# Kernel tuning notes

Measured on AMD Instinct MI355X. Metric: run time of the kernel, lower is better.

The kernel has to match this reference:

```python
import jax, jax.numpy as jnp
import numpy as np

N = 200_000          # active voxels
CIN, COUT = 64, 128  # in_filters, out_filters
GRID = (32, 480, 480)  # sparse spatial shape (D, H, W)
NEG_SLOPE = 0.01     # nn.LeakyReLU default
EPS = 1e-5           # BatchNorm1d default


def _build_nbrs():
    """Build rulebook-style neighbor tables for the two submanifold kernels.

    Returns nbr31 [9, N] for kernel (3,1,3) and nbr13 [9, N] for kernel (1,3,3).
    Entry == N means 'no active neighbor' (maps to a zero pad row).
    """
    rng = np.random.default_rng(0)
    prod = GRID[0] * GRID[1] * GRID[2]
    lin = rng.choice(prod, size=N, replace=False)
    z, y, x = np.unravel_index(lin, GRID)
    lut = np.full(prod, N, dtype=np.int64)
    lut[lin] = np.arange(N)

    def nbrs(offsets):
        out = np.full((len(offsets), N), N, dtype=np.int32)
        for k, (dz, dy, dx) in enumerate(offsets):
            zz, yy, xx = z + dz, y + dy, x + dx
            valid = ((zz >= 0) & (zz < GRID[0]) & (yy >= 0) & (yy < GRID[1])
                     & (xx >= 0) & (xx < GRID[2]))
            l2 = (zz * GRID[1] + yy) * GRID[2] + xx
            out[k, valid] = lut[l2[valid]].astype(np.int32)
        return out

    off31 = [(dz, 0, dx) for dz in (-1, 0, 1) for dx in (-1, 0, 1)]  # (3,1,3)
    off13 = [(0, dy, dx) for dy in (-1, 0, 1) for dx in (-1, 0, 1)]  # (1,3,3)
    return nbrs(off31), nbrs(off13)


def setup_inputs() -> dict:
    key = jax.random.key(0)
    ks = jax.random.split(key, 5)
    nbr31, nbr13 = _build_nbrs()
    s_in = (2.0 / (9 * CIN)) ** 0.5
    s_out = (2.0 / (9 * COUT)) ** 0.5
    ones = jnp.ones((COUT,), jnp.float32)
    zeros = jnp.zeros((COUT,), jnp.float32)
    return {
        "feats": jax.random.normal(ks[0], (N, CIN), jnp.float32),
        "W1": jax.random.normal(ks[1], (9, CIN, COUT), jnp.float32) * s_in,
        "W1_2": jax.random.normal(ks[2], (9, COUT, COUT), jnp.float32) * s_out,
        "W2": jax.random.normal(ks[3], (9, CIN, COUT), jnp.float32) * s_in,
        "W3": jax.random.normal(ks[4], (9, COUT, COUT), jnp.float32) * s_out,
        "g0": ones, "b0": zeros,      # bn0  (init: weight=1, bias=0)
        "g0_2": ones, "b0_2": zeros,  # bn0_2
        "g1": ones, "b1": zeros,      # bn1
        "g2": ones, "b2": zeros,      # bn2
        "nbr31": jnp.asarray(nbr31),
        "nbr13": jnp.asarray(nbr13),
    }


def _subm_conv(f, W, nbr):
    # f [N, Cin], W [9, Cin, Cout], nbr [9, N] -> [N, Cout]
    fp = jnp.concatenate([f, jnp.zeros((1, f.shape[1]), f.dtype)], axis=0)
    g = fp[nbr]  # gather: [9, N, Cin]
    return jnp.einsum("knc,kcd->nd", g, W)


def _lrelu(f):
    return jnp.where(f >= 0, f, NEG_SLOPE * f)


def _bn(f, gamma, beta):
    # BatchNorm1d training-mode batch stats (biased variance) over voxel dim
    m = jnp.mean(f, axis=0)
    v = jnp.mean(jnp.square(f), axis=0) - m * m
    return (f - m) * jax.lax.rsqrt(v + EPS) * gamma + beta


def reference(feats, W1, W1_2, W2, W3, g0, b0, g0_2, b0_2, g1, b1, g2, b2,
              nbr31, nbr13):
    shortcut = _bn(_lrelu(_subm_conv(feats, W1, nbr31)), g0, b0)
    shortcut = _bn(_lrelu(_subm_conv(shortcut, W1_2, nbr13)), g0_2, b0_2)
    resA = _bn(_lrelu(_subm_conv(feats, W2, nbr13)), g1, b1)
    resA = _bn(_lrelu(_subm_conv(resA, W3, nbr31)), g2, b2)
    return resA + shortcut
```

## Files before the change

kernel.cpp:

```cpp
#include <hip/hip_runtime.h>

#define NV 200000
#define NCH 391
#define PCAP 56
#define SNB 256

typedef __attribute__((ext_vector_type(8))) short sh8;
typedef __attribute__((ext_vector_type(4))) float f32x4;
typedef __attribute__((ext_vector_type(2))) unsigned int u32x2;

__device__ inline unsigned short f2bf(float f) {
  unsigned int u = __builtin_bit_cast(unsigned int, f);
  u += 0x7FFFu + ((u >> 16) & 1u);
  return (unsigned short)(u >> 16);
}
__device__ inline float bf2f(unsigned short h) {
  unsigned int u = ((unsigned int)h) << 16;
  return __builtin_bit_cast(float, u);
}
__device__ inline float lrelu(float v) { return v >= 0.f ? v : 0.01f * v; }

__global__ __launch_bounds__(256) void prep_k(
    const float* __restrict__ W1, const float* __restrict__ W12,
    const float* __restrict__ W2, const float* __restrict__ W3,
    unsigned short* __restrict__ T1, unsigned short* __restrict__ T12,
    unsigned short* __restrict__ T2, unsigned short* __restrict__ T3,
    const int* __restrict__ nbr31, const int* __restrict__ nbr13,
    int2* __restrict__ pairs, int* __restrict__ cc) {
  __shared__ int base_s[4];
  __shared__ int run;
  int bx = blockIdx.x;
  if (bx < 1728) {
    int i = bx * 256 + threadIdx.x;
    const float* src;
    unsigned short* dst;
    int cin;
    if (i < 73728) {
      src = W1; dst = T1; cin = 64;
    } else if (i < 147456) {
      src = W2; dst = T2; cin = 64; i -= 73728;
    } else if (i < 294912) {
      src = W12; dst = T12; cin = 128; i -= 147456;
    } else {
      src = W3; dst = T3; cin = 128; i -= 294912;
    }
    const int c = i % cin;
    const int rest = i / cin;
    const int d = rest % 128;
    const int k = rest / 128;
    dst[i] = f2bf(src[((size_t)(k * cin + c)) * 128 + d]);
    return;
  }
  bx -= 1728;
  const int slot = bx / NCH, chunk = bx % NCH;
  const int table = slot >> 3, kk = slot & 7;
  const int k = kk + (kk >= 4);
  const int* nb = (table ? nbr13 : nbr31) + (size_t)k * NV;
  const int tid = threadIdx.x, lane = tid & 63, wv = tid >> 6;
  if (tid == 0) run = 0;
  __syncthreads();
  int2* pw = pairs + (size_t)(slot * NCH + chunk) * PCAP;
#pragma unroll
  for (int i = 0; i < 2; ++i) {
    const int n = chunk * 512 + i * 256 + tid;
    const int val = (n < NV) ? nb[n] : NV;
    const bool valid = (val != NV);
    const unsigned long long m = __ballot(valid);
    const int loff = __popcll(m & ((1ull << lane) - 1ull));
    if (lane == 0) base_s[wv] = __popcll(m);
    __syncthreads();
    int wbase = run;
    for (int w = 0; w < wv; ++w) wbase += base_s[w];
    if (valid) {
      const int pos = wbase + loff;
      if (pos < PCAP) {
        int2 pr;
        pr.x = val;
        pr.y = n;
        pw[pos] = pr;
      }
    }
    __syncthreads();
    if (tid == 0) run += base_s[0] + base_s[1] + base_s[2] + base_s[3];
    __syncthreads();
  }
  if (tid == 0) cc[slot * NCH + chunk] = min(run, PCAP);
}

__global__ __launch_bounds__(256) void center2_k(
    const float* __restrict__ X, const unsigned short* __restrict__ W1t,
    const unsigned short* __restrict__ W2t, unsigned short* __restrict__ Y1,
    unsigned short* __restrict__ Y2) {
  constexpr int CIN = 64, CH = 8;
  __shared__ unsigned short tile[64 * CIN];
  const int tid = threadIdx.x, lane = tid & 63, wv = tid >> 6;
  const int l15 = lane & 15, l4 = lane >> 4;
  const int row0 = blockIdx.x * 64;
  const int js = tid & 7;
#pragma unroll
  for (int i = 0; i < 2; ++i) {
    const int u = i * 256 + tid;
    const int r = u >> 3;
    const f32x4 a = *(const f32x4*)(X + (size_t)(row0 + r) * CIN + js * 8);
    const f32x4 b = *(const f32x4*)(X + (size_t)(row0 + r) * CIN + js * 8 + 4);
    sh8 o;
#pragma unroll
    for (int j = 0; j < 4; ++j) {
      o[j] = (short)f2bf(a[j]);
      o[4 + j] = (short)f2bf(b[j]);
    }
    *(sh8*)(tile + ((size_t)r * CH + (js ^ (r & 7))) * 8) = o;
  }
  __syncthreads();

  f32x4 acc1[2][4], acc2[2][4];
#pragma unroll
  for (int mt = 0; mt < 2; ++mt)
#pragma unroll
    for (int nt = 0; nt < 4; ++nt) {
      acc1[mt][nt] = (f32x4){0.f, 0.f, 0.f, 0.f};
      acc2[mt][nt] = (f32x4){0.f, 0.f, 0.f, 0.f};
    }
  const unsigned short* W1K = W1t + (size_t)(4 * 128) * CIN;
  const unsigned short* W2K = W2t + (size_t)(4 * 128) * CIN;
#pragma unroll
  for (int s = 0; s < 2; ++s) {
    sh8 aw1[2], aw2[2];
#pragma unroll
    for (int mt = 0; mt < 2; ++mt) {
      const int d = (wv * 2 + mt) * 16 + l15;
      aw1[mt] = *(const sh8*)(W1K + (size_t)d * CIN + s * 32 + l4 * 8);
      aw2[mt] = *(const sh8*)(W2K + (size_t)d * CIN + s * 32 + l4 * 8);
    }
#pragma unroll
    for (int nt = 0; nt < 4; ++nt) {
      const int r = nt * 16 + l15;
      const int j = s * 4 + l4;
      const sh8 bx = *(const sh8*)(tile + ((size_t)r * CH + (j ^ (r & 7))) * 8);
#pragma unroll
      for (int mt = 0; mt < 2; ++mt) {
        acc1[mt][nt] =
            __builtin_amdgcn_mfma_f32_16x16x32_bf16(aw1[mt], bx, acc1[mt][nt], 0, 0, 0);
        acc2[mt][nt] =
            __builtin_amdgcn_mfma_f32_16x16x32_bf16(aw2[mt], bx, acc2[mt][nt], 0, 0, 0);
      }
    }
  }
#pragma unroll
  for (int mt = 0; mt < 2; ++mt)
#pragma unroll
    for (int nt = 0; nt < 4; ++nt) {
      const int n = row0 + nt * 16 + l15;
      const int d0 = (wv * 2 + mt) * 16 + l4 * 4;
      u32x2 p1, p2;
      p1[0] = (unsigned)f2bf(acc1[mt][nt][0]) | ((unsigned)f2bf(acc1[mt][nt][1]) << 16);
      p1[1] = (unsigned)f2bf(acc1[mt][nt][2]) | ((unsigned)f2bf(acc1[mt][nt][3]) << 16);
      p2[0] = (unsigned)f2bf(acc2[mt][nt][0]) | ((unsigned)f2bf(acc2[mt][nt][1]) << 16);
      p2[1] = (unsigned)f2bf(acc2[mt][nt][2]) | ((unsigned)f2bf(acc2[mt][nt][3]) << 16);
      *(u32x2*)(Y1 + (size_t)n * 128 + d0) = p1;
      *(u32x2*)(Y2 + (size_t)n * 128 + d0) = p2;
    }
}

__global__ __launch_bounds__(256) void c128_k(
    const unsigned short* __restrict__ X, const unsigned short* __restrict__ Wt,
    const float* __restrict__ abp, unsigned short* __restrict__ Y) {
  constexpr int CIN = 128, CH = 16;
  __shared__ unsigned short tile[64 * CIN];
  const int row0 = blockIdx.x * 64;
  const int tid = threadIdx.x, lane = tid & 63, wv = tid >> 6;
  const int l15 = lane & 15, l4 = lane >> 4;
  const int js = tid & 15;
  const f32x4 aL = *(const f32x4*)(abp + js * 8);
  const f32x4 aH = *(const f32x4*)(abp + js * 8 + 4);
  const f32x4 bL = *(const f32x4*)(abp + 128 + js * 8);
  const f32x4 bH = *(const f32x4*)(abp + 128 + js * 8 + 4);
#pragma unroll
  for (int i = 0; i < 4; ++i) {
    const int u = i * 256 + tid;
    const int r = u >> 4;
    const sh8 v = *(const sh8*)(X + (size_t)(row0 + r) * CIN + js * 8);
    sh8 o;
#pragma unroll
    for (int j = 0; j < 4; ++j) {
      o[j] = (short)f2bf(lrelu(bf2f((unsigned short)v[j])) * aL[j] + bL[j]);
      o[4 + j] = (short)f2bf(lrelu(bf2f((unsigned short)v[4 + j])) * aH[j] + bH[j]);
    }
    *(sh8*)(tile + ((size_t)r * CH + (js ^ (r & 7))) * 8) = o;
  }
  __syncthreads();

  f32x4 acc[2][4];
#pragma unroll
  for (int mt = 0; mt < 2; ++mt)
#pragma unroll
    for (int nt = 0; nt < 4; ++nt) acc[mt][nt] = (f32x4){0.f, 0.f, 0.f, 0.f};

  const unsigned short* WtK = Wt + (size_t)(4 * 128) * CIN;
#pragma unroll
  for (int s = 0; s < 4; ++s) {
    sh8 aw[2];
#pragma unroll
    for (int mt = 0; mt < 2; ++mt) {
      const int d = (wv * 2 + mt) * 16 + l15;
      aw[mt] = *(const sh8*)(WtK + (size_t)d * CIN + s * 32 + l4 * 8);
    }
#pragma unroll
    for (int nt = 0; nt < 4; ++nt) {
      const int r = nt * 16 + l15;
      const int j = s * 4 + l4;
      const sh8 bxv = *(const sh8*)(tile + ((size_t)r * CH + (j ^ (r & 7))) * 8);
#pragma unroll
      for (int mt = 0; mt < 2; ++mt)
        acc[mt][nt] =
            __builtin_amdgcn_mfma_f32_16x16x32_bf16(aw[mt], bxv, acc[mt][nt], 0, 0, 0);
    }
  }
#pragma unroll
  for (int mt = 0; mt < 2; ++mt)
#pragma unroll
    for (int nt = 0; nt < 4; ++nt) {
      const int n = row0 + nt * 16 + l15;
      const int d0 = (wv * 2 + mt) * 16 + l4 * 4;
      u32x2 pk;
      pk[0] = (unsigned)f2bf(acc[mt][nt][0]) | ((unsigned)f2bf(acc[mt][nt][1]) << 16);
      pk[1] = (unsigned)f2bf(acc[mt][nt][2]) | ((unsigned)f2bf(acc[mt][nt][3]) << 16);
      *(u32x2*)(Y + (size_t)n * 128 + d0) = pk;
    }
}

__global__ __launch_bounds__(256) void off64_k(
    const float* __restrict__ X, const unsigned short* __restrict__ T1,
    const unsigned short* __restrict__ T2, const int2* __restrict__ pairs,
    const int* __restrict__ cc, unsigned short* __restrict__ y1,
    unsigned short* __restrict__ y2) {
  constexpr int CIN = 64, CH = 8;
  const int layer = blockIdx.x / NCH, chunk = blockIdx.x % NCH;
  const unsigned short* Wt = layer ? T2 : T1;
  unsigned short* Y = layer ? y2 : y1;
  const int* ccl = cc + layer * 8 * NCH;
  const int2* pl = pairs + (size_t)layer * 8 * NCH * PCAP;
  __shared__ unsigned short tile[64 * CIN];
  __shared__ int sin[64], sout[64];
  const int tid = threadIdx.x, lane = tid & 63, wv = tid >> 6;
  const int l15 = lane & 15, l4 = lane >> 4;
  const int js = tid & 7;

  for (int kk = 0; kk < 8; ++kk) {
    const int n0 = ccl[kk * NCH + chunk];
    if (n0 == 0) continue;
    const int k = kk + (kk >= 4);
    const unsigned short* WtK = Wt + (size_t)k * 128 * CIN;
    __syncthreads();
    if (tid < 64) {
      int2 pr;
      if (tid < n0) pr = pl[(size_t)(kk * NCH + chunk) * PCAP + tid];
      else { pr.x = NV; pr.y = NV; }
      sin[tid] = pr.x;
      sout[tid] = pr.y;
    }
    __syncthreads();
#pragma unroll
    for (int i = 0; i < 2; ++i) {
      const int r = (i * 256 + tid) >> 3;
      const int in = sin[r];
      sh8 o = (sh8){0, 0, 0, 0, 0, 0, 0, 0};
      if (in != NV) {
        const f32x4 a = *(const f32x4*)(X + (size_t)in * CIN + js * 8);
        const f32x4 b = *(const f32x4*)(X + (size_t)in * CIN + js * 8 + 4);
#pragma unroll
        for (int j = 0; j < 4; ++j) {
          o[j] = (short)f2bf(a[j]);
          o[4 + j] = (short)f2bf(b[j]);
        }
      }
      *(sh8*)(tile + ((size_t)r * CH + (js ^ (r & 7))) * 8) = o;
    }
    __syncthreads();

    f32x4 acc[2][4];
#pragma unroll
    for (int mt = 0; mt < 2; ++mt)
#pragma unroll
      for (int nt = 0; nt < 4; ++nt) acc[mt][nt] = (f32x4){0.f, 0.f, 0.f, 0.f};
#pragma unroll
    for (int s = 0; s < 2; ++s) {
      sh8 aw[2];
#pragma unroll
      for (int mt = 0; mt < 2; ++mt) {
        const int d = (wv * 2 + mt) * 16 + l15;
        aw[mt] = *(const sh8*)(WtK + (size_t)d * CIN + s * 32 + l4 * 8);
      }
#pragma unroll
      for (int nt = 0; nt < 4; ++nt) {
        const int r = nt * 16 + l15;
        const int j = s * 4 + l4;
        const sh8 bxv = *(const sh8*)(tile + ((size_t)r * CH + (j ^ (r & 7))) * 8);
#pragma unroll
        for (int mt = 0; mt < 2; ++mt)
          acc[mt][nt] =
              __builtin_amdgcn_mfma_f32_16x16x32_bf16(aw[mt], bxv, acc[mt][nt], 0, 0, 0);
      }
    }
#pragma unroll
    for (int mt = 0; mt < 2; ++mt)
#pragma unroll
      for (int nt = 0; nt < 4; ++nt) {
        const int out = sout[nt * 16 + l15];
        if (out == NV) continue;
        const int d0 = (wv * 2 + mt) * 16 + l4 * 4;
        unsigned short* p = Y + (size_t)out * 128 + d0;
        const u32x2 old = *(const u32x2*)p;
        u32x2 nw;
        nw[0] = (unsigned)f2bf(bf2f((unsigned short)(old[0] & 0xffff)) + acc[mt][nt][0]) |
                ((unsigned)f2bf(bf2f((unsigned short)(old[0] >> 16)) + acc[mt][nt][1]) << 16);
        nw[1] = (unsigned)f2bf(bf2f((unsigned short)(old[1] & 0xffff)) + acc[mt][nt][2]) |
                ((unsigned)f2bf(bf2f((unsigned short)(old[1] >> 16)) + acc[mt][nt][3]) << 16);
        *(u32x2*)p = nw;
      }
  }
}

__global__ __launch_bounds__(256) void off128_k(
    const unsigned short* __restrict__ X, const unsigned short* __restrict__ Wt,
    const int2* __restrict__ pairs_t, const int* __restrict__ cc_t,
    const float* __restrict__ abp, unsigned short* __restrict__ Y) {
  constexpr int CIN = 128, CH = 16;
  const int chunk = blockIdx.x;
  __shared__ unsigned short tile[64 * CIN];
  __shared__ int sin[64], sout[64];
  const int tid = threadIdx.x, lane = tid & 63, wv = tid >> 6;
  const int l15 = lane & 15, l4 = lane >> 4;
  const int js = tid & 15;
  const f32x4 aL = *(const f32x4*)(abp + js * 8);
  const f32x4 aH = *(const f32x4*)(abp + js * 8 + 4);
  const f32x4 bL = *(const f32x4*)(abp + 128 + js * 8);
  const f32x4 bH = *(const f32x4*)(abp + 128 + js * 8 + 4);

  for (int kk = 0; kk < 8; ++kk) {
    const int n0 = cc_t[kk * NCH + chunk];
    if (n0 == 0) continue;
    const int k = kk + (kk >= 4);
    const unsigned short* WtK = Wt + (size_t)k * 128 * CIN;
    __syncthreads();
    if (tid < 64) {
      int2 pr;
      if (tid < n0) pr = pairs_t[(size_t)(kk * NCH + chunk) * PCAP + tid];
      else { pr.x = NV; pr.y = NV; }
      sin[tid] = pr.x;
      sout[tid] = pr.y;
    }
    __syncthreads();
#pragma unroll
    for (int i = 0; i < 4; ++i) {
      const int r = (i * 256 + tid) >> 4;
      const int in = sin[r];
      sh8 o = (sh8){0, 0, 0, 0, 0, 0, 0, 0};
      if (in != NV) {
        const sh8 v = *(const sh8*)(X + (size_t)in * CIN + js * 8);
#pragma unroll
        for (int j = 0; j < 4; ++j) {
          o[j] = (short)f2bf(lrelu(bf2f((unsigned short)v[j])) * aL[j] + bL[j]);
          o[4 + j] = (short)f2bf(lrelu(bf2f((unsigned short)v[4 + j])) * aH[j] + bH[j]);
        }
      }
      *(sh8*)(tile + ((size_t)r * CH + (js ^ (r & 7))) * 8) = o;
    }
    __syncthreads();

    f32x4 acc[2][4];
#pragma unroll
    for (int mt = 0; mt < 2; ++mt)
#pragma unroll
      for (int nt = 0; nt < 4; ++nt) acc[mt][nt] = (f32x4){0.f, 0.f, 0.f, 0.f};
#pragma unroll
    for (int s = 0; s < 4; ++s) {
      sh8 aw[2];
#pragma unroll
      for (int mt = 0; mt < 2; ++mt) {
        const int d = (wv * 2 + mt) * 16 + l15;
        aw[mt] = *(const sh8*)(WtK + (size_t)d * CIN + s * 32 + l4 * 8);
      }
#pragma unroll
      for (int nt = 0; nt < 4; ++nt) {
        const int r = nt * 16 + l15;
        const int j = s * 4 + l4;
        const sh8 bxv = *(const sh8*)(tile + ((size_t)r * CH + (j ^ (r & 7))) * 8);
#pragma unroll
        for (int mt = 0; mt < 2; ++mt)
          acc[mt][nt] =
              __builtin_amdgcn_mfma_f32_16x16x32_bf16(aw[mt], bxv, acc[mt][nt], 0, 0, 0);
      }
    }
#pragma unroll
    for (int mt = 0; mt < 2; ++mt)
#pragma unroll
      for (int nt = 0; nt < 4; ++nt) {
        const int out = sout[nt * 16 + l15];
        if (out == NV) continue;
        const int d0 = (wv * 2 + mt) * 16 + l4 * 4;
        unsigned short* p = Y + (size_t)out * 128 + d0;
        const u32x2 old = *(const u32x2*)p;
        u32x2 nw;
        nw[0] = (unsigned)f2bf(bf2f((unsigned short)(old[0] & 0xffff)) + acc[mt][nt][0]) |
                ((unsigned)f2bf(bf2f((unsigned short)(old[0] >> 16)) + acc[mt][nt][1]) << 16);
        nw[1] = (unsigned)f2bf(bf2f((unsigned short)(old[1] & 0xffff)) + acc[mt][nt][2]) |
                ((unsigned)f2bf(bf2f((unsigned short)(old[1] >> 16)) + acc[mt][nt][3]) << 16);
        *(u32x2*)p = nw;
      }
  }
}

__device__ inline void stats_body(const unsigned short* __restrict__ Y,
                                  float* __restrict__ partial, int b) {
  const int tid = threadIdx.x;
  float s[8], q[8];
#pragma unroll
  for (int j = 0; j < 8; ++j) { s[j] = 0.f; q[j] = 0.f; }
  for (long c = (long)b * 256 + tid; c < (long)NV * 16; c += (long)SNB * 256) {
    const sh8 v = *(const sh8*)(Y + c * 8);
#pragma unroll
    for (int j = 0; j < 8; ++j) {
      const float f = lrelu(bf2f((unsigned short)v[j]));
      s[j] += f;
      q[j] += f * f;
    }
  }
  __shared__ float red[256 * 16];
#pragma unroll
  for (int j = 0; j < 8; ++j) {
    red[tid * 16 + j] = s[j];
    red[tid * 16 + 8 + j] = q[j];
  }
  __syncthreads();
  if (tid < 128) {
    const int g = tid >> 3, j = tid & 7;
    float vs = 0.f, vq = 0.f;
#pragma unroll
    for (int i = 0; i < 16; ++i) {
      vs += red[(g + 16 * i) * 16 + j];
      vq += red[(g + 16 * i) * 16 + 8 + j];
    }
    partial[(size_t)b * 256 + tid] = vs;
    partial[(size_t)b * 256 + 128 + tid] = vq;
  }
}

__global__ __launch_bounds__(256) void stats2_k(const unsigned short* __restrict__ Y1,
                                                const unsigned short* __restrict__ Y2,
                                                float* __restrict__ P1,
                                                float* __restrict__ P2) {
  if (blockIdx.x < SNB) stats_body(Y1, P1, blockIdx.x);
  else stats_body(Y2, P2, blockIdx.x - SNB);
}

__global__ __launch_bounds__(1024) void fin2_k(
    const float* __restrict__ PA, const float* __restrict__ gA,
    const float* __restrict__ btA, float* __restrict__ abA,
    const float* __restrict__ PB, const float* __restrict__ gB,
    const float* __restrict__ btB, float* __restrict__ abB) {
  const float* P = blockIdx.x ? PB : PA;
  const float* g = blockIdx.x ? gB : gA;
  const float* bt = blockIdx.x ? btB : btA;
  float* abo = blockIdx.x ? abB : abA;
  __shared__ float S[1024];
  const int t = threadIdx.x;
  const int c = t & 255, grp = t >> 8;
  float s = 0.f;
#pragma unroll 8
  for (int b = grp * 64; b < grp * 64 + 64; ++b) s += P[(size_t)b * 256 + c];
  S[t] = s;
  __syncthreads();
  if (t < 256) S[t] = S[t] + S[256 + t] + S[512 + t] + S[768 + t];
  __syncthreads();
  if (t < 128) {
    const float m = S[t] * (1.0f / (float)NV);
    const float v = S[128 + t] * (1.0f / (float)NV) - m * m;
    const float a = g[t] * rsqrtf(v + 1e-5f);
    abo[t] = a;
    abo[128 + t] = bt[t] - m * a;
  }
}

__global__ __launch_bounds__(256) void final_k(const unsigned short* __restrict__ y3,
                                               const unsigned short* __restrict__ ysc,
                                               const float* __restrict__ ab3,
                                               const float* __restrict__ ab1,
                                               float* __restrict__ out) {
  const long i = (long)blockIdx.x * 256 + threadIdx.x;
  if (i >= (long)NV * 16) return;
  const long base = i * 8;
  const int c0 = (int)(base & 127);
  const sh8 v3 = *(const sh8*)(y3 + base);
  const sh8 vs = *(const sh8*)(ysc + base);
  const f32x4 a3L = *(const f32x4*)(ab3 + c0);
  const f32x4 a3H = *(const f32x4*)(ab3 + c0 + 4);
  const f32x4 b3L = *(const f32x4*)(ab3 + 128 + c0);
  const f32x4 b3H = *(const f32x4*)(ab3 + 128 + c0 + 4);
  const f32x4 a1L = *(const f32x4*)(ab1 + c0);
  const f32x4 a1H = *(const f32x4*)(ab1 + c0 + 4);
  const f32x4 b1L = *(const f32x4*)(ab1 + 128 + c0);
  const f32x4 b1H = *(const f32x4*)(ab1 + 128 + c0 + 4);
  f32x4 oL, oH;
#pragma unroll
  for (int j = 0; j < 4; ++j) {
    oL[j] = a3L[j] * lrelu(bf2f((unsigned short)v3[j])) + b3L[j] +
            a1L[j] * lrelu(bf2f((unsigned short)vs[j])) + b1L[j];
    oH[j] = a3H[j] * lrelu(bf2f((unsigned short)v3[4 + j])) + b3H[j] +
            a1H[j] * lrelu(bf2f((unsigned short)vs[4 + j])) + b1H[j];
  }
  *(f32x4*)(out + base) = oL;
  *(f32x4*)(out + base + 4) = oH;
}

extern "C" void kernel_launch(void* const* d_in, const int* in_sizes, int n_in,
                              void* d_out, int out_size, void* d_ws, size_t ws_size,
                              hipStream_t stream) {
  const float* feats = (const float*)d_in[0];
  const float* W1 = (const float*)d_in[1];
  const float* W12 = (const float*)d_in[2];
  const float* W2 = (const float*)d_in[3];
  const float* W3 = (const float*)d_in[4];
  const float* g0 = (const float*)d_in[5];
  const float* b0 = (const float*)d_in[6];
  const float* g02 = (const float*)d_in[7];
  const float* b02 = (const float*)d_in[8];
  const float* g1 = (const float*)d_in[9];
  const float* b1 = (const float*)d_in[10];
  const float* g2 = (const float*)d_in[11];
  const float* b2 = (const float*)d_in[12];
  const int* nbr31 = (const int*)d_in[13];
  const int* nbr13 = (const int*)d_in[14];
  float* out = (float*)d_out;

  char* ws = (char*)d_ws;
  size_t off = 0;
  auto alloc = [&](size_t bytes) {
    char* p = ws + off;
    off = (off + bytes + 255) & ~(size_t)255;
    return p;
  };

  unsigned short* T1 = (unsigned short*)alloc((size_t)9 * 128 * 64 * 2);
  unsigned short* T2 = (unsigned short*)alloc((size_t)9 * 128 * 64 * 2);
  unsigned short* T12 = (unsigned short*)alloc((size_t)9 * 128 * 128 * 2);
  unsigned short* T3 = (unsigned short*)alloc((size_t)9 * 128 * 128 * 2);
  unsigned short* y1 = (unsigned short*)alloc((size_t)NV * 128 * 2);
  unsigned short* ysc = (unsigned short*)alloc((size_t)NV * 128 * 2);
  unsigned short* y2 = (unsigned short*)alloc((size_t)NV * 128 * 2);
  float* partA = (float*)alloc((size_t)SNB * 256 * 4);
  float* partB = (float*)alloc((size_t)SNB * 256 * 4);
  float* ab = (float*)alloc(1024 * 4);
  int* cc = (int*)alloc((size_t)16 * NCH * 4);
  int2* pairs = (int2*)alloc((size_t)16 * NCH * PCAP * 8);
  unsigned short* y3 = y1;

  const int2* pairs31 = pairs;
  const int2* pairs13 = pairs + (size_t)8 * NCH * PCAP;
  const int* cc31 = cc;
  const int* cc13 = cc + 8 * NCH;


  prep_k<<<1728 + 16 * NCH, 256, 0, stream>>>(W1, W12, W2, W3, T1, T12, T2, T3,
                                              nbr31, nbr13, pairs, cc);
  center2_k<<<3125, 256, 0, stream>>>(feats, T1, T2, y1, y2);
  off64_k<<<2 * NCH, 256, 0, stream>>>(feats, T1, T2, pairs, cc, y1, y2);
  stats2_k<<<2 * SNB, 256, 0, stream>>>(y1, y2, partA, partB);
  fin2_k<<<2, 1024, 0, stream>>>(partA, g0, b0, ab + 0, partB, g1, b1, ab + 256);
  c128_k<<<3125, 256, 0, stream>>>(y1, T12, ab + 0, ysc);
  off128_k<<<NCH, 256, 0, stream>>>(y1, T12, pairs13, cc13, ab + 0, ysc);
  c128_k<<<3125, 256, 0, stream>>>(y2, T3, ab + 256, y3);
  off128_k<<<NCH, 256, 0, stream>>>(y2, T3, pairs31, cc31, ab + 256, y3);
  stats2_k<<<2 * SNB, 256, 0, stream>>>(ysc, y3, partA, partB);
  fin2_k<<<2, 1024, 0, stream>>>(partA, g02, b02, ab + 512, partB, g2, b2, ab + 768);
  final_k<<<12500, 256, 0, stream>>>(y3, ysc, ab + 768, ab + 512, out);
}
```

Before: 311.8 us.

## Fuse BatchNorm statistics into conv epilogues and drop separate stats passes

Removes the two stats2 kernels that re-read the full bf16 activations. The center-tap GEMM kernels now emit per-block sums and sums of squares of the leaky-ReLU outputs. The off-center scatter kernels emit the delta each updated value contributes. fin2 reduces over all these partial rows. Output stores are staged through LDS for coalesced 16-byte writes, and weight transposition uses LDS tiles in fewer blocks. The trade-off is that stats now come from fp32 values before bf16 rounding, and fin2 has many more partial rows to reduce.

```diff
diff --git a/kernel.cpp b/kernel.cpp
--- a/kernel.cpp
+++ b/kernel.cpp
@@ -3,7 +3,8 @@
 #define NV 200000
 #define NCH 391
 #define PCAP 56
-#define SNB 256
+#define CG 3125
+#define PN 3516
 
 typedef __attribute__((ext_vector_type(8))) short sh8;
 typedef __attribute__((ext_vector_type(4))) float f32x4;
@@ -27,36 +28,44 @@
     unsigned short* __restrict__ T2, unsigned short* __restrict__ T3,
     const int* __restrict__ nbr31, const int* __restrict__ nbr13,
     int2* __restrict__ pairs, int* __restrict__ cc) {
+  __shared__ unsigned short lt[64 * 130];
   __shared__ int base_s[4];
   __shared__ int run;
   int bx = blockIdx.x;
-  if (bx < 1728) {
-    int i = bx * 256 + threadIdx.x;
+  const int tid = threadIdx.x;
+  if (bx < 36) {
     const float* src;
     unsigned short* dst;
-    int cin;
-    if (i < 73728) {
-      src = W1; dst = T1; cin = 64;
-    } else if (i < 147456) {
-      src = W2; dst = T2; cin = 64; i -= 73728;
-    } else if (i < 294912) {
-      src = W12; dst = T12; cin = 128; i -= 147456;
-    } else {
-      src = W3; dst = T3; cin = 128; i -= 294912;
-    }
-    const int c = i % cin;
-    const int rest = i / cin;
-    const int d = rest % 128;
-    const int k = rest / 128;
-    dst[i] = f2bf(src[((size_t)(k * cin + c)) * 128 + d]);
+    int cin, k;
+    if (bx < 9) { src = W1; dst = T1; cin = 64; k = bx; }
+    else if (bx < 18) { src = W2; dst = T2; cin = 64; k = bx - 9; }
+    else if (bx < 27) { src = W12; dst = T12; cin = 128; k = bx - 18; }
+    else { src = W3; dst = T3; cin = 128; k = bx - 27; }
+    src += (size_t)k * cin * 128;
+    dst += (size_t)k * 128 * cin;
+    const int cmask = cin - 1;
+    const int csh = (cin == 64) ? 6 : 7;
+    for (int h = 0; h < 2; ++h) {
+      if (h) __syncthreads();
+      const int tot = cin * 64;
+      for (int e = tid; e < tot; e += 256) {
+        const int c = e >> 6, dd = e & 63;
+        lt[dd * 130 + c] = f2bf(src[c * 128 + h * 64 + dd]);
+      }
+      __syncthreads();
+      for (int o = tid; o < tot; o += 256) {
+        const int dl = o >> csh, c = o & cmask;
+        dst[(size_t)(h * 64 + dl) * cin + c] = lt[dl * 130 + c];
+      }
+    }
     return;
   }
-  bx -= 1728;
+  bx -= 36;
   const int slot = bx / NCH, chunk = bx % NCH;
   const int table = slot >> 3, kk = slot & 7;
   const int k = kk + (kk >= 4);
   const int* nb = (table ? nbr13 : nbr31) + (size_t)k * NV;
-  const int tid = threadIdx.x, lane = tid & 63, wv = tid >> 6;
+  const int lane = tid & 63, wv = tid >> 6;
   if (tid == 0) run = 0;
   __syncthreads();
   int2* pw = pairs + (size_t)(slot * NCH + chunk) * PCAP;
@@ -87,20 +96,66 @@
   if (tid == 0) cc[slot * NCH + chunk] = min(run, PCAP);
 }
 
+#define STATS_EMIT(ACC, PART)                                                   \
+  {                                                                             \
+    f32x4 ssum[2], ssq[2];                                                      \
+    _Pragma("unroll") for (int mt = 0; mt < 2; ++mt) {                          \
+      ssum[mt] = (f32x4){0.f, 0.f, 0.f, 0.f};                                   \
+      ssq[mt] = (f32x4){0.f, 0.f, 0.f, 0.f};                                    \
+      _Pragma("unroll") for (int nt = 0; nt < 4; ++nt)                          \
+          _Pragma("unroll") for (int q = 0; q < 4; ++q) {                       \
+        const float f = lrelu(ACC[mt][nt][q]);                                  \
+        ssum[mt][q] += f;                                                       \
+        ssq[mt][q] += f * f;                                                    \
+      }                                                                         \
+      _Pragma("unroll") for (int off = 1; off < 16; off <<= 1)                  \
+          _Pragma("unroll") for (int q = 0; q < 4; ++q) {                       \
+        ssum[mt][q] += __shfl_xor(ssum[mt][q], off);                            \
+        ssq[mt][q] += __shfl_xor(ssq[mt][q], off);                              \
+      }                                                                         \
+      if (l15 == 0) {                                                           \
+        const int d0 = (wv * 2 + mt) * 16 + l4 * 4;                             \
+        *(f32x4*)(PART + (size_t)blockIdx.x * 256 + d0) = ssum[mt];             \
+        *(f32x4*)(PART + (size_t)blockIdx.x * 256 + 128 + d0) = ssq[mt];        \
+      }                                                                         \
+    }                                                                           \
+  }
+
+#define TILE_OUT(ACC, YPTR)                                                     \
+  {                                                                             \
+    __syncthreads();                                                            \
+    _Pragma("unroll") for (int mt = 0; mt < 2; ++mt)                            \
+        _Pragma("unroll") for (int nt = 0; nt < 4; ++nt) {                      \
+      u32x2 pk;                                                                 \
+      pk[0] = (unsigned)f2bf(ACC[mt][nt][0]) |                                  \
+              ((unsigned)f2bf(ACC[mt][nt][1]) << 16);                           \
+      pk[1] = (unsigned)f2bf(ACC[mt][nt][2]) |                                  \
+              ((unsigned)f2bf(ACC[mt][nt][3]) << 16);                           \
+      *(u32x2*)(&lds[(nt * 16 + l15) * 136 + (wv * 2 + mt) * 16 + l4 * 4]) = pk;\
+    }                                                                           \
+    __syncthreads();                                                            \
+    _Pragma("unroll") for (int j = 0; j < 4; ++j) {                             \
+      const int row = j * 16 + (tid >> 4);                                      \
+      const int c16 = tid & 15;                                                 \
+      const sh8 v = *(const sh8*)(&lds[row * 136 + c16 * 8]);                   \
+      *(sh8*)(YPTR + (size_t)(row0 + row) * 128 + c16 * 8) = v;                 \
+    }                                                                           \
+  }
+
 __global__ __launch_bounds__(256) void center2_k(
     const float* __restrict__ X, const unsigned short* __restrict__ W1t,
     const unsigned short* __restrict__ W2t, unsigned short* __restrict__ Y1,
-    unsigned short* __restrict__ Y2) {
+    unsigned short* __restrict__ Y2, float* __restrict__ PA,
+    float* __restrict__ PB) {
   constexpr int CIN = 64, CH = 8;
-  __shared__ unsigned short tile[64 * CIN];
+  __shared__ unsigned short lds[64 * 136];
   const int tid = threadIdx.x, lane = tid & 63, wv = tid >> 6;
   const int l15 = lane & 15, l4 = lane >> 4;
   const int row0 = blockIdx.x * 64;
   const int js = tid & 7;
 #pragma unroll
   for (int i = 0; i < 2; ++i) {
-    const int u = i * 256 + tid;
-    const int r = u >> 3;
+    const int r = (i * 256 + tid) >> 3;
     const f32x4 a = *(const f32x4*)(X + (size_t)(row0 + r) * CIN + js * 8);
     const f32x4 b = *(const f32x4*)(X + (size_t)(row0 + r) * CIN + js * 8 + 4);
     sh8 o;
@@ -109,7 +164,7 @@
       o[j] = (short)f2bf(a[j]);
       o[4 + j] = (short)f2bf(b[j]);
     }
-    *(sh8*)(tile + ((size_t)r * CH + (js ^ (r & 7))) * 8) = o;
+    *(sh8*)(lds + ((size_t)r * CH + (js ^ (r & 7))) * 8) = o;
   }
   __syncthreads();
 
@@ -136,7 +191,7 @@
     for (int nt = 0; nt < 4; ++nt) {
       const int r = nt * 16 + l15;
       const int j = s * 4 + l4;
-      const sh8 bx = *(const sh8*)(tile + ((size_t)r * CH + (j ^ (r & 7))) * 8);
+      const sh8 bx = *(const sh8*)(lds + ((size_t)r * CH + (j ^ (r & 7))) * 8);
 #pragma unroll
       for (int mt = 0; mt < 2; ++mt) {
         acc1[mt][nt] =
@@ -146,27 +201,19 @@
       }
     }
   }
-#pragma unroll
-  for (int mt = 0; mt < 2; ++mt)
-#pragma unroll
-    for (int nt = 0; nt < 4; ++nt) {
-      const int n = row0 + nt * 16 + l15;
-      const int d0 = (wv * 2 + mt) * 16 + l4 * 4;
-      u32x2 p1, p2;
-      p1[0] = (unsigned)f2bf(acc1[mt][nt][0]) | ((unsigned)f2bf(acc1[mt][nt][1]) << 16);
-      p1[1] = (unsigned)f2bf(acc1[mt][nt][2]) | ((unsigned)f2bf(acc1[mt][nt][3]) << 16);
-      p2[0] = (unsigned)f2bf(acc2[mt][nt][0]) | ((unsigned)f2bf(acc2[mt][nt][1]) << 16);
-      p2[1] = (unsigned)f2bf(acc2[mt][nt][2]) | ((unsigned)f2bf(acc2[mt][nt][3]) << 16);
-      *(u32x2*)(Y1 + (size_t)n * 128 + d0) = p1;
-      *(u32x2*)(Y2 + (size_t)n * 128 + d0) = p2;
-    }
+  STATS_EMIT(acc1, PA)
+  STATS_EMIT(acc2, PB)
+  TILE_OUT(acc1, Y1)
+  __syncthreads();
+  TILE_OUT(acc2, Y2)
 }
 
 __global__ __launch_bounds__(256) void c128_k(
     const unsigned short* __restrict__ X, const unsigned short* __restrict__ Wt,
-    const float* __restrict__ abp, unsigned short* __restrict__ Y) {
+    const float* __restrict__ abp, unsigned short* __restrict__ Y,
+    float* __restrict__ PART) {
   constexpr int CIN = 128, CH = 16;
-  __shared__ unsigned short tile[64 * CIN];
+  __shared__ unsigned short lds[64 * 136];
   const int row0 = blockIdx.x * 64;
   const int tid = threadIdx.x, lane = tid & 63, wv = tid >> 6;
   const int l15 = lane & 15, l4 = lane >> 4;
@@ -177,8 +224,7 @@
   const f32x4 bH = *(const f32x4*)(abp + 128 + js * 8 + 4);
 #pragma unroll
   for (int i = 0; i < 4; ++i) {
-    const int u = i * 256 + tid;
-    const int r = u >> 4;
+    const int r = (i * 256 + tid) >> 4;
     const sh8 v = *(const sh8*)(X + (size_t)(row0 + r) * CIN + js * 8);
     sh8 o;
 #pragma unroll
@@ -186,7 +232,7 @@
       o[j] = (short)f2bf(lrelu(bf2f((unsigned short)v[j])) * aL[j] + bL[j]);
       o[4 + j] = (short)f2bf(lrelu(bf2f((unsigned short)v[4 + j])) * aH[j] + bH[j]);
     }
-    *(sh8*)(tile + ((size_t)r * CH + (js ^ (r & 7))) * 8) = o;
+    *(sh8*)(lds + ((size_t)r * CH + (js ^ (r & 7))) * 8) = o;
   }
   __syncthreads();
 
@@ -209,35 +255,28 @@
     for (int nt = 0; nt < 4; ++nt) {
       const int r = nt * 16 + l15;
       const int j = s * 4 + l4;
-      const sh8 bxv = *(const sh8*)(tile + ((size_t)r * CH + (j ^ (r & 7))) * 8);
+      const sh8 bxv = *(const sh8*)(lds + ((size_t)r * CH + (j ^ (r & 7))) * 8);
 #pragma unroll
       for (int mt = 0; mt < 2; ++mt)
         acc[mt][nt] =
             __builtin_amdgcn_mfma_f32_16x16x32_bf16(aw[mt], bxv, acc[mt][nt], 0, 0, 0);
     }
   }
-#pragma unroll
-  for (int mt = 0; mt < 2; ++mt)
-#pragma unroll
-    for (int nt = 0; nt < 4; ++nt) {
-      const int n = row0 + nt * 16 + l15;
-      const int d0 = (wv * 2 + mt) * 16 + l4 * 4;
-      u32x2 pk;
-      pk[0] = (unsigned)f2bf(acc[mt][nt][0]) | ((unsigned)f2bf(acc[mt][nt][1]) << 16);
-      pk[1] = (unsigned)f2bf(acc[mt][nt][2]) | ((unsigned)f2bf(acc[mt][nt][3]) << 16);
-      *(u32x2*)(Y + (size_t)n * 128 + d0) = pk;
-    }
+  STATS_EMIT(acc, PART)
+  TILE_OUT(acc, Y)
 }
 
 __global__ __launch_bounds__(256) void off64_k(
     const float* __restrict__ X, const unsigned short* __restrict__ T1,
     const unsigned short* __restrict__ T2, const int2* __restrict__ pairs,
     const int* __restrict__ cc, unsigned short* __restrict__ y1,
-    unsigned short* __restrict__ y2) {
+    unsigned short* __restrict__ y2, float* __restrict__ PA,
+    float* __restrict__ PB) {
   constexpr int CIN = 64, CH = 8;
   const int layer = blockIdx.x / NCH, chunk = blockIdx.x % NCH;
   const unsigned short* Wt = layer ? T2 : T1;
   unsigned short* Y = layer ? y2 : y1;
+  float* PD = layer ? PB : PA;
   const int* ccl = cc + layer * 8 * NCH;
   const int2* pl = pairs + (size_t)layer * 8 * NCH * PCAP;
   __shared__ unsigned short tile[64 * CIN];
@@ -245,6 +284,12 @@
   const int tid = threadIdx.x, lane = tid & 63, wv = tid >> 6;
   const int l15 = lane & 15, l4 = lane >> 4;
   const int js = tid & 7;
+  f32x4 ds[2], dq[2];
+#pragma unroll
+  for (int mt = 0; mt < 2; ++mt) {
+    ds[mt] = (f32x4){0.f, 0.f, 0.f, 0.f};
+    dq[mt] = (f32x4){0.f, 0.f, 0.f, 0.f};
+  }
 
   for (int kk = 0; kk < 8; ++kk) {
     const int n0 = ccl[kk * NCH + chunk];
@@ -312,19 +357,45 @@
         unsigned short* p = Y + (size_t)out * 128 + d0;
         const u32x2 old = *(const u32x2*)p;
         u32x2 nw;
-        nw[0] = (unsigned)f2bf(bf2f((unsigned short)(old[0] & 0xffff)) + acc[mt][nt][0]) |
-                ((unsigned)f2bf(bf2f((unsigned short)(old[0] >> 16)) + acc[mt][nt][1]) << 16);
-        nw[1] = (unsigned)f2bf(bf2f((unsigned short)(old[1] & 0xffff)) + acc[mt][nt][2]) |
-                ((unsigned)f2bf(bf2f((unsigned short)(old[1] >> 16)) + acc[mt][nt][3]) << 16);
+        float of[4], sf[4];
+        of[0] = bf2f((unsigned short)(old[0] & 0xffff));
+        of[1] = bf2f((unsigned short)(old[0] >> 16));
+        of[2] = bf2f((unsigned short)(old[1] & 0xffff));
+        of[3] = bf2f((unsigned short)(old[1] >> 16));
+#pragma unroll
+        for (int q = 0; q < 4; ++q) {
+          sf[q] = of[q] + acc[mt][nt][q];
+          const float ln = lrelu(sf[q]), lo = lrelu(of[q]);
+          ds[mt][q] += ln - lo;
+          dq[mt][q] += ln * ln - lo * lo;
+        }
+        nw[0] = (unsigned)f2bf(sf[0]) | ((unsigned)f2bf(sf[1]) << 16);
+        nw[1] = (unsigned)f2bf(sf[2]) | ((unsigned)f2bf(sf[3]) << 16);
         *(u32x2*)p = nw;
       }
+  }
+#pragma unroll
+  for (int mt = 0; mt < 2; ++mt) {
+#pragma unroll
+    for (int off = 1; off < 16; off <<= 1)
+#pragma unroll
+      for (int q = 0; q < 4; ++q) {
+        ds[mt][q] += __shfl_xor(ds[mt][q], off);
+        dq[mt][q] += __shfl_xor(dq[mt][q], off);
+      }
+    if (l15 == 0) {
+      const int d0 = (wv * 2 + mt) * 16 + l4 * 4;
+      *(f32x4*)(PD + (size_t)(CG + chunk) * 256 + d0) = ds[mt];
+      *(f32x4*)(PD + (size_t)(CG + chunk) * 256 + 128 + d0) = dq[mt];
+    }
   }
 }
 
 __global__ __launch_bounds__(256) void off128_k(
     const unsigned short* __restrict__ X, const unsigned short* __restrict__ Wt,
     const int2* __restrict__ pairs_t, const int* __restrict__ cc_t,
-    const float* __restrict__ abp, unsigned short* __restrict__ Y) {
+    const float* __restrict__ abp, unsigned short* __restrict__ Y,
+    float* __restrict__ PD) {
   constexpr int CIN = 128, CH = 16;
   const int chunk = blockIdx.x;
   __shared__ unsigned short tile[64 * CIN];
@@ -336,6 +407,12 @@
   const f32x4 aH = *(const f32x4*)(abp + js * 8 + 4);
   const f32x4 bL = *(const f32x4*)(abp + 128 + js * 8);
   const f32x4 bH = *(const f32x4*)(abp + 128 + js * 8 + 4);
+  f32x4 ds[2], dq[2];
+#pragma unroll
+  for (int mt = 0; mt < 2; ++mt) {
+    ds[mt] = (f32x4){0.f, 0.f, 0.f, 0.f};
+    dq[mt] = (f32x4){0.f, 0.f, 0.f, 0.f};
+  }
 
   for (int kk = 0; kk < 8; ++kk) {
     const int n0 = cc_t[kk * NCH + chunk];
@@ -402,56 +479,38 @@
         unsigned short* p = Y + (size_t)out * 128 + d0;
         const u32x2 old = *(const u32x2*)p;
         u32x2 nw;
-        nw[0] = (unsigned)f2bf(bf2f((unsigned short)(old[0] & 0xffff)) + acc[mt][nt][0]) |
-                ((unsigned)f2bf(bf2f((unsigned short)(old[0] >> 16)) + acc[mt][nt][1]) << 16);
-        nw[1] = (unsigned)f2bf(bf2f((unsigned short)(old[1] & 0xffff)) + acc[mt][nt][2]) |
-                ((unsigned)f2bf(bf2f((unsigned short)(old[1] >> 16)) + acc[mt][nt][3]) << 16);
+        float of[4], sf[4];
+        of[0] = bf2f((unsigned short)(old[0] & 0xffff));
+        of[1] = bf2f((unsigned short)(old[0] >> 16));
+        of[2] = bf2f((unsigned short)(old[1] & 0xffff));
+        of[3] = bf2f((unsigned short)(old[1] >> 16));
+#pragma unroll
+        for (int q = 0; q < 4; ++q) {
+          sf[q] = of[q] + acc[mt][nt][q];
+          const float ln = lrelu(sf[q]), lo = lrelu(of[q]);
+          ds[mt][q] += ln - lo;
+          dq[mt][q] += ln * ln - lo * lo;
+        }
+        nw[0] = (unsigned)f2bf(sf[0]) | ((unsigned)f2bf(sf[1]) << 16);
+        nw[1] = (unsigned)f2bf(sf[2]) | ((unsigned)f2bf(sf[3]) << 16);
         *(u32x2*)p = nw;
       }
   }
-}
-
-__device__ inline void stats_body(const unsigned short* __restrict__ Y,
-                                  float* __restrict__ partial, int b) {
-  const int tid = threadIdx.x;
-  float s[8], q[8];
-#pragma unroll
-  for (int j = 0; j < 8; ++j) { s[j] = 0.f; q[j] = 0.f; }
-  for (long c = (long)b * 256 + tid; c < (long)NV * 16; c += (long)SNB * 256) {
-    const sh8 v = *(const sh8*)(Y + c * 8);
-#pragma unroll
-    for (int j = 0; j < 8; ++j) {
-      const float f = lrelu(bf2f((unsigned short)v[j]));
-      s[j] += f;
-      q[j] += f * f;
-    }
-  }
-  __shared__ float red[256 * 16];
-#pragma unroll
-  for (int j = 0; j < 8; ++j) {
-    red[tid * 16 + j] = s[j];
-    red[tid * 16 + 8 + j] = q[j];
-  }
-  __syncthreads();
-  if (tid < 128) {
-    const int g = tid >> 3, j = tid & 7;
-    float vs = 0.f, vq = 0.f;
-#pragma unroll
-    for (int i = 0; i < 16; ++i) {
-      vs += red[(g + 16 * i) * 16 + j];
-      vq += red[(g + 16 * i) * 16 + 8 + j];
-    }
-    partial[(size_t)b * 256 + tid] = vs;
-    partial[(size_t)b * 256 + 128 + tid] = vq;
-  }
-}
-
-__global__ __launch_bounds__(256) void stats2_k(const unsigned short* __restrict__ Y1,
-                                                const unsigned short* __restrict__ Y2,
-                                                float* __restrict__ P1,
-                                                float* __restrict__ P2) {
-  if (blockIdx.x < SNB) stats_body(Y1, P1, blockIdx.x);
-  else stats_body(Y2, P2, blockIdx.x - SNB);
+#pragma unroll
+  for (int mt = 0; mt < 2; ++mt) {
+#pragma unroll
+    for (int off = 1; off < 16; off <<= 1)
+#pragma unroll
+      for (int q = 0; q < 4; ++q) {
+        ds[mt][q] += __shfl_xor(ds[mt][q], off);
+        dq[mt][q] += __shfl_xor(dq[mt][q], off);
+      }
+    if (l15 == 0) {
+      const int d0 = (wv * 2 + mt) * 16 + l4 * 4;
+      *(f32x4*)(PD + (size_t)(CG + chunk) * 256 + d0) = ds[mt];
+      *(f32x4*)(PD + (size_t)(CG + chunk) * 256 + 128 + d0) = dq[mt];
+    }
+  }
 }
 
 __global__ __launch_bounds__(1024) void fin2_k(
@@ -467,8 +526,7 @@
   const int t = threadIdx.x;
   const int c = t & 255, grp = t >> 8;
   float s = 0.f;
-#pragma unroll 8
-  for (int b = grp * 64; b < grp * 64 + 64; ++b) s += P[(size_t)b * 256 + c];
+  for (int b = grp; b < PN; b += 4) s += P[(size_t)b * 256 + c];
   S[t] = s;
   __syncthreads();
   if (t < 256) S[t] = S[t] + S[256 + t] + S[512 + t] + S[768 + t];
@@ -548,8 +606,8 @@
   unsigned short* y1 = (unsigned short*)alloc((size_t)NV * 128 * 2);
   unsigned short* ysc = (unsigned short*)alloc((size_t)NV * 128 * 2);
   unsigned short* y2 = (unsigned short*)alloc((size_t)NV * 128 * 2);
-  float* partA = (float*)alloc((size_t)SNB * 256 * 4);
-  float* partB = (float*)alloc((size_t)SNB * 256 * 4);
+  float* PA = (float*)alloc((size_t)PN * 256 * 4);
+  float* PB = (float*)alloc((size_t)PN * 256 * 4);
   float* ab = (float*)alloc(1024 * 4);
   int* cc = (int*)alloc((size_t)16 * NCH * 4);
   int2* pairs = (int2*)alloc((size_t)16 * NCH * PCAP * 8);
@@ -561,17 +619,15 @@
   const int* cc13 = cc + 8 * NCH;
 
 
-  prep_k<<<1728 + 16 * NCH, 256, 0, stream>>>(W1, W12, W2, W3, T1, T12, T2, T3,
-                                              nbr31, nbr13, pairs, cc);
-  center2_k<<<3125, 256, 0, stream>>>(feats, T1, T2, y1, y2);
-  off64_k<<<2 * NCH, 256, 0, stream>>>(feats, T1, T2, pairs, cc, y1, y2);
-  stats2_k<<<2 * SNB, 256, 0, stream>>>(y1, y2, partA, partB);
-  fin2_k<<<2, 1024, 0, stream>>>(partA, g0, b0, ab + 0, partB, g1, b1, ab + 256);
-  c128_k<<<3125, 256, 0, stream>>>(y1, T12, ab + 0, ysc);
-  off128_k<<<NCH, 256, 0, stream>>>(y1, T12, pairs13, cc13, ab + 0, ysc);
-  c128_k<<<3125, 256, 0, stream>>>(y2, T3, ab + 256, y3);
-  off128_k<<<NCH, 256, 0, stream>>>(y2, T3, pairs31, cc31, ab + 256, y3);
-  stats2_k<<<2 * SNB, 256, 0, stream>>>(ysc, y3, partA, partB);
-  fin2_k<<<2, 1024, 0, stream>>>(partA, g02, b02, ab + 512, partB, g2, b2, ab + 768);
+  prep_k<<<36 + 16 * NCH, 256, 0, stream>>>(W1, W12, W2, W3, T1, T12, T2, T3,
+                                            nbr31, nbr13, pairs, cc);
+  center2_k<<<CG, 256, 0, stream>>>(feats, T1, T2, y1, y2, PA, PB);
+  off64_k<<<2 * NCH, 256, 0, stream>>>(feats, T1, T2, pairs, cc, y1, y2, PA, PB);
+  fin2_k<<<2, 1024, 0, stream>>>(PA, g0, b0, ab + 0, PB, g1, b1, ab + 256);
+  c128_k<<<CG, 256, 0, stream>>>(y1, T12, ab + 0, ysc, PA);
+  off128_k<<<NCH, 256, 0, stream>>>(y1, T12, pairs13, cc13, ab + 0, ysc, PA);
+  c128_k<<<CG, 256, 0, stream>>>(y2, T3, ab + 256, y3, PB);
+  off128_k<<<NCH, 256, 0, stream>>>(y2, T3, pairs31, cc31, ab + 256, y3, PB);
+  fin2_k<<<2, 1024, 0, stream>>>(PA, g02, b02, ab + 512, PB, g2, b2, ab + 768);
   final_k<<<12500, 256, 0, stream>>>(y3, ysc, ab + 768, ab + 512, out);
 }
```

New measurement: 730.7 us. +134.4%, slower.
